# Performance work log

Hardware: AMD Instinct MI355X
Metric: run time of the kernel (lower is better)

Reference implementation:

```python
import jax, jax.numpy as jnp
import numpy as np

N_NODES = 100000
N_EDGES = 3200000


def setup_inputs() -> dict:
    key = jax.random.key(0)
    ks = jax.random.split(key, 16)
    inp = {
        "noisy_coords": jax.random.normal(ks[0], (N_NODES, 3), dtype=jnp.float32),
        "atom_types": jax.random.randint(ks[1], (N_NODES,), 0, 2),
        "edge_index": jax.random.randint(ks[2], (2, N_EDGES), 0, N_NODES),
        "emb": jax.random.normal(ks[3], (2, 3), dtype=jnp.float32),
    }
    # GCNConv weights: 6->32->64->64->32->3 (hidden_dim=64)
    dims = [(6, 32), (32, 64), (64, 64), (64, 32), (32, 3)]
    for i, (din, dout) in enumerate(dims, start=1):
        inp[f"W{i}"] = jax.random.normal(ks[3 + i], (din, dout), dtype=jnp.float32) / np.sqrt(din).astype(np.float32)
        inp[f"b{i}"] = jnp.zeros((dout,), dtype=jnp.float32)
    return inp


def _gcn_conv(x, W, b, src, dst, norm, n):
    # GCNConv: X @ W, then symmetric-normalized scatter-add over edges, then bias.
    h = x @ W                       # [N, dout]
    msg = h[src] * norm[:, None]    # gather + edge normalization  [E+N, dout]
    return jax.ops.segment_sum(msg, dst, num_segments=n) + b


def reference(noisy_coords, atom_types, edge_index, emb,
              W1, b1, W2, b2, W3, b3, W4, b4, W5, b5):
    n = noisy_coords.shape[0]
    loop = jnp.arange(n)
    # PyG GCNConv adds self loops and uses deg^{-1/2} (A+I) deg^{-1/2} normalization
    src = jnp.concatenate([edge_index[0], loop])
    dst = jnp.concatenate([edge_index[1], loop])
    deg = jax.ops.segment_sum(jnp.ones(src.shape[0], dtype=jnp.float32), dst, num_segments=n)
    dinv = jnp.where(deg > 0, jax.lax.rsqrt(deg), 0.0)
    norm = dinv[src] * dinv[dst]    # [E+N]

    x = jnp.concatenate([noisy_coords, emb[atom_types]], axis=1)  # [N, 6]
    x = jax.nn.relu(_gcn_conv(x, W1, b1, src, dst, norm, n))
    x = jax.nn.relu(_gcn_conv(x, W2, b2, src, dst, norm, n))
    x = jax.nn.relu(_gcn_conv(x, W3, b3, src, dst, norm, n))
    x = jax.nn.relu(_gcn_conv(x, W4, b4, src, dst, norm, n))
    x = _gcn_conv(x, W5, b5, src, dst, norm, n)  # final layer: no relu
    return x
```

## Files before the change

kernel.cpp:

```cpp
#include <hip/hip_runtime.h>
#include <hip/hip_fp16.h>

#define NBLK_BIN 512
#define NBKT 196
#define BWIN 512
#define CAP 64
#define SCAP 40
#define PHASE 2048
#define OVF_CAP 65536

typedef unsigned int uint;

union U32H2 { uint u; __half2 h; };

__device__ inline float2 h2_to_f2(uint u) {
    U32H2 c; c.u = u;
    return __half22float2(c.h);
}
__device__ inline uint f2_to_h2(float a, float b) {
    U32H2 c; c.h = __floats2half2_rn(a, b);
    return c.u;
}

__global__ __launch_bounds__(512) void bin_kernel(const int* __restrict__ src,
                                                  const int* __restrict__ dst,
                                                  int2* __restrict__ pairs,
                                                  int* __restrict__ blkcnt,
                                                  int2* __restrict__ ovf,
                                                  int* __restrict__ ovf_cnt, int e) {
    __shared__ __align__(16) int2 stage[NBKT][SCAP];
    __shared__ int lcnt[NBKT];
    __shared__ int gcur[NBKT];
    int blk = blockIdx.x, tid = threadIdx.x;
    for (int t = tid; t < NBKT; t += 512) { lcnt[t] = 0; gcur[t] = 0; }
    __syncthreads();
    int chunk = (e + NBLK_BIN - 1) / NBLK_BIN;
    int base = blk * chunk;
    int end = min(e, base + chunk);
    for (int ib = base; ib < end; ib += PHASE) {
        int iend = min(end, ib + PHASE);
        for (int i = ib + tid; i < iend; i += 512) {
            int s = src[i], d = dst[i];
            int b = d >> 9;
            int pos = atomicAdd(&lcnt[b], 1);
            if (pos < SCAP) stage[b][pos] = make_int2(s, d);
            else { int p = atomicAdd(ovf_cnt, 1); if (p < OVF_CAP) ovf[p] = make_int2(s, d); }
        }
        __syncthreads();
        if (tid < NBKT) {
            int b = tid;
            int c = min(lcnt[b], SCAP);
            int nl = c >> 3;
            int g = gcur[b];
            int4* cell = (int4*)(pairs + ((size_t)blk * NBKT + b) * CAP);
            const int4* st = (const int4*)&stage[b][0];
            for (int l = 0; l < nl; ++l) {
                if (g + 8 <= CAP) {
                    int o = g >> 1;
                    cell[o]     = st[4 * l];
                    cell[o + 1] = st[4 * l + 1];
                    cell[o + 2] = st[4 * l + 2];
                    cell[o + 3] = st[4 * l + 3];
                    g += 8;
                } else {
                    int p = atomicAdd(ovf_cnt, 8);
                    for (int k = 0; k < 8; ++k)
                        if (p + k < OVF_CAP) ovf[p + k] = stage[b][8 * l + k];
                }
            }
            gcur[b] = g;
            int rem = c & 7;
            for (int k = 0; k < rem; ++k) stage[b][k] = stage[b][8 * nl + k];
            lcnt[b] = rem;
        }
        __syncthreads();
    }
    if (tid < NBKT) {
        int b = tid;
        int rem = min(lcnt[b], SCAP);
        int g = gcur[b];
        if (rem > 0) {
            if (g + 8 <= CAP) {
                int4* cell = (int4*)(pairs + ((size_t)blk * NBKT + b) * CAP);
                const int4* st = (const int4*)&stage[b][0];
                int o = g >> 1;
                cell[o] = st[0]; cell[o + 1] = st[1]; cell[o + 2] = st[2]; cell[o + 3] = st[3];
                g += rem;
            } else if (g + rem <= CAP) {
                for (int k = 0; k < rem; ++k)
                    pairs[((size_t)blk * NBKT + b) * CAP + g + k] = stage[b][k];
                g += rem;
            } else {
                int p = atomicAdd(ovf_cnt, rem);
                for (int k = 0; k < rem; ++k)
                    if (p + k < OVF_CAP) ovf[p + k] = stage[b][k];
            }
        }
        blkcnt[blk * NBKT + b] = g;
    }
}

__global__ __launch_bounds__(512) void fill_kernel(const int2* __restrict__ pairs,
                                                   const int* __restrict__ blkcnt,
                                                   const int2* __restrict__ ovf,
                                                   const int* __restrict__ ovf_cnt,
                                                   int* __restrict__ gcounter,
                                                   int* __restrict__ srcs,
                                                   int* __restrict__ cnt,
                                                   int* __restrict__ rowptr,
                                                   float* __restrict__ dinv, int n) {
    __shared__ int lc[BWIN];
    __shared__ int ps[BWIN];
    __shared__ int sm[NBLK_BIN];
    __shared__ int gbase_s;
    int b = blockIdx.x, tid = threadIdx.x;
    int nbase = b << 9;
    lc[tid] = 0;
    for (int t = tid; t < NBLK_BIN; t += 512) sm[t] = blkcnt[t * NBKT + b];
    __syncthreads();
    int wave = tid >> 6, lane = tid & 63;
    for (int blk = wave; blk < NBLK_BIN; blk += 8) {
        int m = sm[blk];
        const int2* p = pairs + ((size_t)blk * NBKT + b) * CAP;
        for (int i = lane; i < m; i += 64) atomicAdd(&lc[p[i].y - nbase], 1);
    }
    int novf = min(*ovf_cnt, OVF_CAP);
    for (int i = tid; i < novf; i += 512) {
        int d = ovf[i].y;
        if ((d >> 9) == b) atomicAdd(&lc[d - nbase], 1);
    }
    __syncthreads();
    int myc = lc[tid];
    ps[tid] = myc;
    __syncthreads();
    for (int off = 1; off < 512; off <<= 1) {
        int t = (tid >= off) ? ps[tid - off] : 0;
        __syncthreads();
        ps[tid] += t;
        __syncthreads();
    }
    if (tid == 511) gbase_s = atomicAdd(gcounter, ps[511]);
    __syncthreads();
    int ex = ps[tid] - myc;
    int gbase = gbase_s;
    int vtx = nbase + tid;
    if (vtx < n) {
        cnt[vtx] = myc;
        rowptr[vtx] = gbase + ex;
        dinv[vtx] = rsqrtf(1.0f + (float)myc);
    }
    __syncthreads();
    lc[tid] = ex;
    __syncthreads();
    for (int blk = wave; blk < NBLK_BIN; blk += 8) {
        int m = sm[blk];
        const int2* p = pairs + ((size_t)blk * NBKT + b) * CAP;
        for (int i = lane; i < m; i += 64) {
            int2 e2 = p[i];
            int o = atomicAdd(&lc[e2.y - nbase], 1);
            srcs[gbase + o] = e2.x;
        }
    }
    for (int i = tid; i < novf; i += 512) {
        int2 e2 = ovf[i];
        if ((e2.y >> 9) == b) {
            int o = atomicAdd(&lc[e2.y - nbase], 1);
            srcs[gbase + o] = e2.x;
        }
    }
}


__global__ __launch_bounds__(256) void build_x0_h_kernel(const float* __restrict__ coords,
                                                         const int* __restrict__ at,
                                                         const float* __restrict__ emb,
                                                         const float* __restrict__ dinv,
                                                         uint* __restrict__ x, int n) {
    int v = blockIdx.x * 256 + threadIdx.x;
    if (v >= n) return;
    float dv = dinv[v];
    float c0 = coords[3 * v + 0] * dv;
    float c1 = coords[3 * v + 1] * dv;
    float c2 = coords[3 * v + 2] * dv;
    int t = at[v];
    float e0 = emb[3 * t + 0] * dv;
    float e1 = emb[3 * t + 1] * dv;
    float e2 = emb[3 * t + 2] * dv;
    uint* row = x + (size_t)v * 4;
    row[0] = f2_to_h2(c0, c1);
    row[1] = f2_to_h2(c2, e0);
    row[2] = f2_to_h2(e1, e2);
    row[3] = 0;
}

template <int FPH2, bool HAS_BIAS, bool RELU>
__global__ __launch_bounds__(256) void agg_h_kernel(const uint* __restrict__ in,
                                                    const float* __restrict__ dinv,
                                                    const int* __restrict__ rowptr,
                                                    const int* __restrict__ cnt,
                                                    const int* __restrict__ srcs,
                                                    const float* __restrict__ bias,
                                                    uint* __restrict__ out, int n) {
    int gid = blockIdx.x * 256 + threadIdx.x;
    int v = gid / FPH2, j2 = gid % FPH2;
    if (v >= n) return;
    float2 s0 = h2_to_f2(in[(size_t)v * FPH2 + j2]);
    float accx = s0.x, accy = s0.y;
    int start = rowptr[v];
    int len = cnt[v];
    int k = 0;
    for (; k + 4 <= len; k += 4) {
        int sA = srcs[start + k];
        int sB = srcs[start + k + 1];
        int sC = srcs[start + k + 2];
        int sD = srcs[start + k + 3];
        float2 fA = h2_to_f2(in[(size_t)sA * FPH2 + j2]);
        float2 fB = h2_to_f2(in[(size_t)sB * FPH2 + j2]);
        float2 fC = h2_to_f2(in[(size_t)sC * FPH2 + j2]);
        float2 fD = h2_to_f2(in[(size_t)sD * FPH2 + j2]);
        accx += (fA.x + fB.x) + (fC.x + fD.x);
        accy += (fA.y + fB.y) + (fC.y + fD.y);
    }
    for (; k < len; ++k) {
        int s = srcs[start + k];
        float2 f = h2_to_f2(in[(size_t)s * FPH2 + j2]);
        accx += f.x; accy += f.y;
    }
    float dv = dinv[v];
    accx *= dv; accy *= dv;
    if (HAS_BIAS) { accx += bias[2 * j2]; accy += bias[2 * j2 + 1]; }
    if (RELU) { accx = fmaxf(accx, 0.0f); accy = fmaxf(accy, 0.0f); }
    out[(size_t)v * FPH2 + j2] = f2_to_h2(accx, accy);
}

template <int DIN, int DOUT, int DOUTH2, bool HAS_BIAS, bool RELU, bool SCALE, bool OUTF>
__global__ __launch_bounds__(256) void gemm_h_kernel(const uint* __restrict__ xin,
                                                     const float* __restrict__ W,
                                                     const float* __restrict__ bias,
                                                     const float* __restrict__ dinv,
                                                     void* __restrict__ xout,
                                                     int istride_u, int ostride, int n) {
    __shared__ float wlds[DIN * DOUT];
    for (int i = threadIdx.x; i < DIN * DOUT; i += 256) wlds[i] = W[i];
    __syncthreads();
    int gid = blockIdx.x * 256 + threadIdx.x;
    int v = gid / DOUTH2, j2 = gid % DOUTH2;
    if (v >= n) return;
    int j1 = 2 * j2;
    const uint* xr = xin + (size_t)v * istride_u;
    float acc0 = 0.0f, acc1 = 0.0f;
#pragma unroll
    for (int ku = 0; ku < DIN / 2; ++ku) {
        float2 xf = h2_to_f2(xr[ku]);
        int k = 2 * ku;
        acc0 = fmaf(xf.x, wlds[k * DOUT + j1], acc0);
        acc0 = fmaf(xf.y, wlds[(k + 1) * DOUT + j1], acc0);
        if (j1 + 1 < DOUT) {
            acc1 = fmaf(xf.x, wlds[k * DOUT + j1 + 1], acc1);
            acc1 = fmaf(xf.y, wlds[(k + 1) * DOUT + j1 + 1], acc1);
        }
    }
    if (HAS_BIAS) {
        acc0 += bias[j1];
        if (j1 + 1 < DOUT) acc1 += bias[j1 + 1];
    }
    if (RELU) { acc0 = fmaxf(acc0, 0.0f); acc1 = fmaxf(acc1, 0.0f); }
    if (SCALE) { float dv = dinv[v]; acc0 *= dv; acc1 *= dv; }
    if (OUTF) {
        float* o = (float*)xout + (size_t)v * ostride;
        o[j1] = acc0;
        if (j1 + 1 < DOUT) o[j1 + 1] = acc1;
    } else {
        ((uint*)xout)[(size_t)v * ostride + j2] = f2_to_h2(acc0, acc1);
    }
}

template <int F, int FP, bool HAS_BIAS, bool RELU>
__global__ __launch_bounds__(256) void agg_f_kernel(const float* __restrict__ in,
                                                    const float* __restrict__ dinv,
                                                    const int* __restrict__ rowptr,
                                                    const int* __restrict__ cnt,
                                                    const int* __restrict__ srcs,
                                                    const float* __restrict__ b,
                                                    float* __restrict__ out,
                                                    int istride, int ostride, int n) {
    int gid = blockIdx.x * 256 + threadIdx.x;
    int v = gid / FP, j = gid % FP;
    if (v >= n || j >= F) return;
    float dv = dinv[v];
    int start = rowptr[v];
    int len = cnt[v];
    float acc = in[(size_t)v * istride + j];
    int k = 0;
    for (; k + 4 <= len; k += 4) {
        int s0 = srcs[start + k];
        int s1 = srcs[start + k + 1];
        int s2 = srcs[start + k + 2];
        int s3 = srcs[start + k + 3];
        float a0 = in[(size_t)s0 * istride + j];
        float a1 = in[(size_t)s1 * istride + j];
        float a2 = in[(size_t)s2 * istride + j];
        float a3 = in[(size_t)s3 * istride + j];
        acc += (a0 + a1) + (a2 + a3);
    }
    for (; k < len; ++k) acc += in[(size_t)srcs[start + k] * istride + j];
    float val = acc * dv;
    if (HAS_BIAS) val += b[j];
    if (RELU) val = fmaxf(val, 0.0f);
    out[(size_t)v * ostride + j] = val;
}


extern "C" void kernel_launch(void* const* d_in, const int* in_sizes, int n_in,
                              void* d_out, int out_size, void* d_ws, size_t ws_size,
                              hipStream_t stream) {
    const float* coords = (const float*)d_in[0];
    const int* at       = (const int*)d_in[1];
    const int* ei       = (const int*)d_in[2];
    const float* emb    = (const float*)d_in[3];
    const float* W1 = (const float*)d_in[4];  const float* b1 = (const float*)d_in[5];
    const float* W2 = (const float*)d_in[6];  const float* b2 = (const float*)d_in[7];
    const float* W3 = (const float*)d_in[8];  const float* b3 = (const float*)d_in[9];
    const float* W4 = (const float*)d_in[10]; const float* b4 = (const float*)d_in[11];
    const float* W5 = (const float*)d_in[12]; const float* b5 = (const float*)d_in[13];
    float* out = (float*)d_out;

    const int n = in_sizes[0] / 3;
    const int e = in_sizes[2] / 2;
    const int* src = ei;
    const int* dst = ei + e;

    char* ws = (char*)d_ws;
    size_t off = 0;
    float* dinv   = (float*)(ws + off); off += (size_t)n * 4;
    int*   cnt    = (int*)(ws + off);   off += (size_t)n * 4;
    int*   rowptr = (int*)(ws + off);   off += (size_t)n * 4;
    int*   ctrs   = (int*)(ws + off);   off += 64;
    int*   blkcnt = (int*)(ws + off);   off += (size_t)NBLK_BIN * NBKT * 4;
    int2*  ovf    = (int2*)(ws + off);  off += (size_t)OVF_CAP * 8;
    int*   srcs   = (int*)(ws + off);   off += (size_t)e * 4;
    char*  alias  = ws + off;
    int2*  pairs  = (int2*)alias;
    uint*  A_h    = (uint*)alias;
    uint*  B_h    = A_h + (size_t)n * 32;
    float* B_f    = (float*)(B_h + (size_t)n * 32);

    int nb = (n + 255) / 256;

    hipMemsetAsync(ctrs, 0, 64, stream);
    bin_kernel<<<NBLK_BIN, 512, 0, stream>>>(src, dst, pairs, blkcnt, ovf, ctrs, e);
    fill_kernel<<<NBKT, 512, 0, stream>>>(pairs, blkcnt, ovf, ctrs, ctrs + 1,
                                          srcs, cnt, rowptr, dinv, n);

    build_x0_h_kernel<<<nb, 256, 0, stream>>>(coords, at, emb, dinv, A_h, n);

    auto blocks = [](long long threads) { return (int)((threads + 255) / 256); };

    agg_h_kernel<4, false, false><<<blocks((long long)n * 4), 256, 0, stream>>>(
        A_h, dinv, rowptr, cnt, srcs, nullptr, B_h, n);
    gemm_h_kernel<6, 32, 16, true, true, true, false><<<blocks((long long)n * 16), 256, 0, stream>>>(
        B_h, W1, b1, dinv, A_h, 4, 16, n);

    agg_h_kernel<16, false, false><<<blocks((long long)n * 16), 256, 0, stream>>>(
        A_h, dinv, rowptr, cnt, srcs, nullptr, B_h, n);
    gemm_h_kernel<32, 64, 32, true, true, true, false><<<blocks((long long)n * 32), 256, 0, stream>>>(
        B_h, W2, b2, dinv, A_h, 16, 32, n);

    agg_h_kernel<32, false, false><<<blocks((long long)n * 32), 256, 0, stream>>>(
        A_h, dinv, rowptr, cnt, srcs, nullptr, B_h, n);
    gemm_h_kernel<64, 64, 32, true, true, false, false><<<blocks((long long)n * 32), 256, 0, stream>>>(
        B_h, W3, b3, dinv, A_h, 32, 32, n);

    gemm_h_kernel<64, 32, 16, false, false, true, false><<<blocks((long long)n * 16), 256, 0, stream>>>(
        A_h, W4, nullptr, dinv, B_h, 32, 16, n);
    agg_h_kernel<16, true, true><<<blocks((long long)n * 16), 256, 0, stream>>>(
        B_h, dinv, rowptr, cnt, srcs, b4, A_h, n);

    gemm_h_kernel<32, 3, 2, false, false, true, true><<<blocks((long long)n * 2), 256, 0, stream>>>(
        A_h, W5, nullptr, dinv, B_f, 16, 4, n);
    agg_f_kernel<3, 4, true, false><<<blocks((long long)n * 4), 256, 0, stream>>>(
        B_f, dinv, rowptr, cnt, srcs, b5, out, 4, 3, n);
}
```

Measured before the change: 484.3 us.

## Order CSR segments deterministically by bucket prefix and widen binning blocks

The fill kernel no longer takes its output base from a global atomic counter. Each bucket block now computes its base as a prefix sum over the per-block counts of all lower buckets plus overflow entries, which makes the CSR layout ordered by destination. The bin and fill kernels move to 1024-thread blocks, the number of binning blocks is halved and the per-cell capacity is doubled. This is meant to improve the locality of srcs and rowptr for the aggregation kernels and to use more threads per CU, at the cost of redundant prefix reads of blkcnt that grow with the bucket index.

```diff
diff --git a/kernel.cpp b/kernel.cpp
--- a/kernel.cpp
+++ b/kernel.cpp
@@ -1,14 +1,15 @@
 #include <hip/hip_runtime.h>
 #include <hip/hip_fp16.h>
 
-#define NBLK_BIN 512
+#define NBLK_BIN 256
 #define NBKT 196
 #define BWIN 512
-#define CAP 64
+#define CAP 128
 #define SCAP 40
 #define PHASE 2048
 #define OVF_CAP 65536
 
+
 typedef unsigned int uint;
 
 union U32H2 { uint u; __half2 h; };
@@ -22,24 +23,24 @@
     return c.u;
 }
 
-__global__ __launch_bounds__(512) void bin_kernel(const int* __restrict__ src,
-                                                  const int* __restrict__ dst,
-                                                  int2* __restrict__ pairs,
-                                                  int* __restrict__ blkcnt,
-                                                  int2* __restrict__ ovf,
-                                                  int* __restrict__ ovf_cnt, int e) {
+__global__ __launch_bounds__(1024) void bin_kernel(const int* __restrict__ src,
+                                                   const int* __restrict__ dst,
+                                                   int2* __restrict__ pairs,
+                                                   int* __restrict__ blkcnt,
+                                                   int2* __restrict__ ovf,
+                                                   int* __restrict__ ovf_cnt, int e) {
     __shared__ __align__(16) int2 stage[NBKT][SCAP];
     __shared__ int lcnt[NBKT];
     __shared__ int gcur[NBKT];
     int blk = blockIdx.x, tid = threadIdx.x;
-    for (int t = tid; t < NBKT; t += 512) { lcnt[t] = 0; gcur[t] = 0; }
+    for (int t = tid; t < NBKT; t += 1024) { lcnt[t] = 0; gcur[t] = 0; }
     __syncthreads();
     int chunk = (e + NBLK_BIN - 1) / NBLK_BIN;
     int base = blk * chunk;
     int end = min(e, base + chunk);
     for (int ib = base; ib < end; ib += PHASE) {
         int iend = min(end, ib + PHASE);
-        for (int i = ib + tid; i < iend; i += 512) {
+        for (int i = ib + tid; i < iend; i += 1024) {
             int s = src[i], d = dst[i];
             int b = d >> 9;
             int pos = atomicAdd(&lcnt[b], 1);
@@ -100,59 +101,73 @@
     }
 }
 
-__global__ __launch_bounds__(512) void fill_kernel(const int2* __restrict__ pairs,
-                                                   const int* __restrict__ blkcnt,
-                                                   const int2* __restrict__ ovf,
-                                                   const int* __restrict__ ovf_cnt,
-                                                   int* __restrict__ gcounter,
-                                                   int* __restrict__ srcs,
-                                                   int* __restrict__ cnt,
-                                                   int* __restrict__ rowptr,
-                                                   float* __restrict__ dinv, int n) {
+__global__ __launch_bounds__(1024) void fill_kernel(const int2* __restrict__ pairs,
+                                                    const int* __restrict__ blkcnt,
+                                                    const int2* __restrict__ ovf,
+                                                    const int* __restrict__ ovf_cnt,
+                                                    int* __restrict__ srcs,
+                                                    int* __restrict__ cnt,
+                                                    int* __restrict__ rowptr,
+                                                    float* __restrict__ dinv, int n) {
     __shared__ int lc[BWIN];
     __shared__ int ps[BWIN];
     __shared__ int sm[NBLK_BIN];
     __shared__ int gbase_s;
     int b = blockIdx.x, tid = threadIdx.x;
     int nbase = b << 9;
-    lc[tid] = 0;
-    for (int t = tid; t < NBLK_BIN; t += 512) sm[t] = blkcnt[t * NBKT + b];
-    __syncthreads();
+    if (tid < BWIN) lc[tid] = 0;
+    for (int t = tid; t < NBLK_BIN; t += 1024) sm[t] = blkcnt[t * NBKT + b];
+    if (tid == 0) gbase_s = 0;
+    __syncthreads();
+    int novf = min(*ovf_cnt, OVF_CAP);
+    {
+        long long tot = (long long)NBLK_BIN * b;
+        int lsum = 0;
+        for (long long j = tid; j < tot; j += 1024) {
+            int blk = (int)(j / b);
+            int bp  = (int)(j - (long long)blk * b);
+            lsum += blkcnt[blk * NBKT + bp];
+        }
+        for (int i = tid; i < novf; i += 1024)
+            if ((ovf[i].y >> 9) < b) ++lsum;
+        for (int o = 32; o > 0; o >>= 1) lsum += __shfl_down(lsum, o, 64);
+        if ((tid & 63) == 0 && lsum != 0) atomicAdd(&gbase_s, lsum);
+    }
     int wave = tid >> 6, lane = tid & 63;
-    for (int blk = wave; blk < NBLK_BIN; blk += 8) {
+    for (int blk = wave; blk < NBLK_BIN; blk += 16) {
         int m = sm[blk];
         const int2* p = pairs + ((size_t)blk * NBKT + b) * CAP;
         for (int i = lane; i < m; i += 64) atomicAdd(&lc[p[i].y - nbase], 1);
     }
-    int novf = min(*ovf_cnt, OVF_CAP);
-    for (int i = tid; i < novf; i += 512) {
+    for (int i = tid; i < novf; i += 1024) {
         int d = ovf[i].y;
         if ((d >> 9) == b) atomicAdd(&lc[d - nbase], 1);
     }
     __syncthreads();
-    int myc = lc[tid];
-    ps[tid] = myc;
-    __syncthreads();
-    for (int off = 1; off < 512; off <<= 1) {
-        int t = (tid >= off) ? ps[tid - off] : 0;
+    int myc = (tid < BWIN) ? lc[tid] : 0;
+    if (tid < BWIN) ps[tid] = myc;
+    __syncthreads();
+    for (int off = 1; off < BWIN; off <<= 1) {
+        int t = 0;
+        if (tid < BWIN && tid >= off) t = ps[tid - off];
         __syncthreads();
-        ps[tid] += t;
+        if (tid < BWIN) ps[tid] += t;
         __syncthreads();
     }
-    if (tid == 511) gbase_s = atomicAdd(gcounter, ps[511]);
-    __syncthreads();
-    int ex = ps[tid] - myc;
     int gbase = gbase_s;
-    int vtx = nbase + tid;
-    if (vtx < n) {
-        cnt[vtx] = myc;
-        rowptr[vtx] = gbase + ex;
-        dinv[vtx] = rsqrtf(1.0f + (float)myc);
-    }
-    __syncthreads();
-    lc[tid] = ex;
-    __syncthreads();
-    for (int blk = wave; blk < NBLK_BIN; blk += 8) {
+    if (tid < BWIN) {
+        int ex = ps[tid] - myc;
+        int vtx = nbase + tid;
+        if (vtx < n) {
+            cnt[vtx] = myc;
+            rowptr[vtx] = gbase + ex;
+            dinv[vtx] = rsqrtf(1.0f + (float)myc);
+        }
+    }
+    __syncthreads();
+    if (tid < BWIN) lc[tid] = ps[tid] - myc;
+    __syncthreads();
+    for (int blk = wave; blk < NBLK_BIN; blk += 16) {
         int m = sm[blk];
         const int2* p = pairs + ((size_t)blk * NBKT + b) * CAP;
         for (int i = lane; i < m; i += 64) {
@@ -161,7 +176,7 @@
             srcs[gbase + o] = e2.x;
         }
     }
-    for (int i = tid; i < novf; i += 512) {
+    for (int i = tid; i < novf; i += 1024) {
         int2 e2 = ovf[i];
         if ((e2.y >> 9) == b) {
             int o = atomicAdd(&lc[e2.y - nbase], 1);
@@ -348,9 +363,8 @@
     int nb = (n + 255) / 256;
 
     hipMemsetAsync(ctrs, 0, 64, stream);
-    bin_kernel<<<NBLK_BIN, 512, 0, stream>>>(src, dst, pairs, blkcnt, ovf, ctrs, e);
-    fill_kernel<<<NBKT, 512, 0, stream>>>(pairs, blkcnt, ovf, ctrs, ctrs + 1,
-                                          srcs, cnt, rowptr, dinv, n);
+    bin_kernel<<<NBLK_BIN, 1024, 0, stream>>>(src, dst, pairs, blkcnt, ovf, ctrs, e);
+    fill_kernel<<<NBKT, 1024, 0, stream>>>(pairs, blkcnt, ovf, ctrs, srcs, cnt, rowptr, dinv, n);
 
     build_x0_h_kernel<<<nb, 256, 0, stream>>>(coords, at, emb, dinv, A_h, n);
 
```

Result: faster. 470.7 us (-2.8%).
